# Kernel tuning notes

Measured on AMD Instinct MI355X. Metric: run time of the kernel, lower is better.

Reference implementation:

```python
import jax, jax.numpy as jnp
import numpy as np

BN_EPS = 1e-5

def setup_inputs() -> dict:
    key = jax.random.key(0)
    k1, k2, k3 = jax.random.split(key, 3)
    B, E, Cin, Cout, K, H, W = 32, 8, 64, 64, 3, 112, 112
    x = jax.random.normal(k1, (B, Cin, H, W), dtype=jnp.float32)
    routing_weight = jax.random.uniform(k2, (B, E), dtype=jnp.float32)
    experts = jax.random.normal(k3, (E, Cout, Cin, K, K), dtype=jnp.float32) * 0.05
    gamma = jnp.ones((Cout,), dtype=jnp.float32)
    beta = jnp.zeros((Cout,), dtype=jnp.float32)
    return {"x": x, "routing_weight": routing_weight, "experts": experts,
            "gamma": gamma, "beta": beta}

def reference(x, routing_weight, experts, gamma, beta):
    B, Cin, H, W = x.shape
    E, Cout, _, K, _ = experts.shape
    # Per-sample weighted combination of expert kernels: (B, Cout, Cin, K, K)
    kernels = jnp.einsum('be,eoihw->boihw', routing_weight, experts)
    # Batched conv via grouped-conv trick: groups = B
    xg = x.reshape(1, B * Cin, H, W)
    wg = kernels.reshape(B * Cout, Cin, K, K)
    pad = (K - 1) // 2
    out = jax.lax.conv_general_dilated(
        xg, wg,
        window_strides=(1, 1),
        padding=[(pad, pad), (pad, pad)],
        dimension_numbers=('NCHW', 'OIHW', 'NCHW'),
        feature_group_count=B,
    )
    out = out.reshape(B, Cout, H, W)
    # BatchNorm (training-mode batch stats, biased variance) + ReLU6
    mean = jnp.mean(out, axis=(0, 2, 3), keepdims=True)
    var = jnp.mean(jnp.square(out - mean), axis=(0, 2, 3), keepdims=True)
    g = gamma.reshape(1, -1, 1, 1)
    b = beta.reshape(1, -1, 1, 1)
    y = (out - mean) * jax.lax.rsqrt(var + BN_EPS) * g + b
    return jnp.clip(y, 0.0, 6.0)
```

## Files before the change

kernel.cpp:

```cpp
#include <hip/hip_runtime.h>
#include <stdint.h>

#define BN_EPS 1e-5f

typedef __attribute__((ext_vector_type(8))) short bf16x8;
typedef __attribute__((ext_vector_type(4))) float f32x4;

#define B_    32
#define E_    8
#define CIN   64
#define COUT  64
#define H_    112
#define W_    112
#define HW    (H_*W_)
#define HP    114
#define WP    114
#define CI    32
#define NCHUNK 2
#define NBLK  (B_*56)
#define XT_BC_BYTES (HP*WP*CI*2)
#define XT_BYTES    (B_*NCHUNK*XT_BC_BYTES)
#define KER_BC_BYTES (9*COUT*CI*2)
#define KER_OFF     XT_BYTES
#define KER_BYTES   (B_*NCHUNK*KER_BC_BYTES)
#define PART_OFF    (KER_OFF + KER_BYTES)
#define PART_BYTES  (NBLK*128*4)
#define STATS_OFF   (PART_OFF + PART_BYTES)
#define CVOUT_OFF   (STATS_OFF + 512)
#define CVOUT_BYTES ((long)B_*COUT*HW*2)
#define WS_NEED_BF16 (CVOUT_OFF + CVOUT_BYTES)

static __device__ __forceinline__ unsigned short f2bf(float f) {
    unsigned int u = __float_as_uint(f);
    unsigned int r = (u + 0x7fffu + ((u >> 16) & 1u)) >> 16;
    return (unsigned short)r;
}
static __device__ __forceinline__ float bf2f(unsigned short u) {
    return __uint_as_float(((unsigned int)u) << 16);
}

static __device__ __forceinline__ void gld16(void* lds, const void* g) {
    __builtin_amdgcn_global_load_lds(
        (const __attribute__((address_space(1))) void*)g,
        (__attribute__((address_space(3))) void*)lds, 16, 0, 0);
}

__global__ __launch_bounds__(256)
void prep_kernel(const float* __restrict__ rw,
                 const float* __restrict__ experts,
                 const float* __restrict__ x,
                 char* __restrict__ ws) {
    __shared__ float lds[16 * 289];
    int t = threadIdx.x;

    if (blockIdx.x < 256) {
        int blk = blockIdx.x;
        int oq  = blk & 3;
        int bc  = blk >> 2;
        int c = bc & 1, b = bc >> 1;

        float w[E_];
#pragma unroll
        for (int e = 0; e < E_; e++) w[e] = rw[b * E_ + e];

#pragma unroll
        for (int k = 0; k < 18; k++) {
            int idx = k * 256 + t;
            int o16 = idx / 288;
            int r   = idx - o16 * 288;
            long base = (long)(oq * 16 + o16) * 576 + c * 288 + r;
            float s = 0.f;
#pragma unroll
            for (int e = 0; e < E_; e++) s += w[e] * experts[(long)e * 36864 + base];
            lds[o16 * 289 + r] = s;
        }
        __syncthreads();

        char* kb = ws + (long)KER_OFF + (long)bc * KER_BC_BYTES;
        for (int u = t; u < 576; u += 256) {
            int slot = u & 3;
            int o16  = (u >> 2) & 15;
            int s    = u >> 6;
            float v[8];
#pragma unroll
            for (int j = 0; j < 8; j++) v[j] = lds[o16 * 289 + (slot * 8 + j) * 9 + s];
            uint4 p;
            p.x = (unsigned)f2bf(v[0]) | ((unsigned)f2bf(v[1]) << 16);
            p.y = (unsigned)f2bf(v[2]) | ((unsigned)f2bf(v[3]) << 16);
            p.z = (unsigned)f2bf(v[4]) | ((unsigned)f2bf(v[5]) << 16);
            p.w = (unsigned)f2bf(v[6]) | ((unsigned)f2bf(v[7]) << 16);
            *(uint4*)(kb + s * (COUT * CI * 2) + (oq * 16 + o16) * (CI * 2) + slot * 16) = p;
        }
    } else {
        int blk = blockIdx.x - 256;
        int hp  = blk % HP;
        int bc  = blk / HP;
        int c = bc & 1, b = bc >> 1;
        int h = hp - 1;
        bool border = (h < 0 || h >= H_);

        if (!border) {
            const float* src = x + ((long)(b * CIN + c * CI)) * HW + (long)h * W_;
#pragma unroll
            for (int idx = t; idx < 896; idx += 256) {
                int ch = idx / 28, col = idx % 28;
                float4 v = *(const float4*)(src + (long)ch * HW + col * 4);
                *(float4*)&lds[ch * 112 + col * 4] = v;
            }
        }
        __syncthreads();

        char* dst = ws + (long)bc * XT_BC_BYTES + (long)hp * (WP * CI * 2);
        for (int u = t; u < 456; u += 256) {
            int slot = u & 3, wp = u >> 2;
            int w = wp - 1;
            uint4 p = {0u, 0u, 0u, 0u};
            if (!border && w >= 0 && w < W_) {
                int ch0 = slot * 8;
                float v0 = lds[(ch0 + 0) * 112 + w], v1 = lds[(ch0 + 1) * 112 + w];
                float v2 = lds[(ch0 + 2) * 112 + w], v3 = lds[(ch0 + 3) * 112 + w];
                float v4 = lds[(ch0 + 4) * 112 + w], v5 = lds[(ch0 + 5) * 112 + w];
                float v6 = lds[(ch0 + 6) * 112 + w], v7 = lds[(ch0 + 7) * 112 + w];
                p.x = (unsigned)f2bf(v0) | ((unsigned)f2bf(v1) << 16);
                p.y = (unsigned)f2bf(v2) | ((unsigned)f2bf(v3) << 16);
                p.z = (unsigned)f2bf(v4) | ((unsigned)f2bf(v5) << 16);
                p.w = (unsigned)f2bf(v6) | ((unsigned)f2bf(v7) << 16);
            }
            int sw = slot ^ ((wp >> 1) & 3);
            *(uint4*)(dst + wp * 64 + sw * 16) = p;
        }
    }
}

template<bool BF16OUT>
__global__ __launch_bounds__(256)
void conv_kernel(const char* __restrict__ ws, void* __restrict__ outp,
                 float* __restrict__ partial) {
    __shared__ uint4 xs4[1888];
    char* xs = (char*)xs4;

    int blk0 = blockIdx.x;
    int blk  = (blk0 & 7) * 224 + (blk0 >> 3);
    int b  = blk / 56;
    int rb = blk % 56;
    int h0 = rb * 2;

    int tid  = threadIdx.x;
    int wave = tid >> 6;
    int lane = tid & 63;
    int l15  = lane & 15;
    int g    = lane >> 4;
    int row  = h0 + (wave >> 1);
    int obase = (wave & 1) * 32;
    int rhalf = wave >> 1;

    int swk[3];
#pragma unroll
    for (int kw = 0; kw < 3; kw++)
        swk[kw] = (g ^ (((l15 + kw) >> 1) & 3)) * 16 + (l15 + kw) * 64;

    f32x4 acc[7][2];
#pragma unroll
    for (int mt = 0; mt < 7; mt++)
#pragma unroll
        for (int nh = 0; nh < 2; nh++)
            acc[mt][nh] = (f32x4){0.f, 0.f, 0.f, 0.f};

    for (int c = 0; c < NCHUNK; c++) {
        int bc = b * 2 + c;
        if (c) __syncthreads();
        const char* src = ws + (long)bc * XT_BC_BYTES + (long)h0 * (WP * CI * 2);
#pragma unroll
        for (int i = 0; i < 7; i++) {
            int off = i * 4096 + wave * 1024;
            gld16(xs + off, src + off + lane * 16);
        }
        if (wave == 0) {
            int off = 7 * 4096;
            gld16(xs + off, src + off + lane * 16);
        }
        const char* kbase = ws + (long)KER_OFF + (long)bc * KER_BC_BYTES;
        bf16x8 bb[9][2];
#pragma unroll
        for (int s = 0; s < 9; s++)
#pragma unroll
            for (int nh = 0; nh < 2; nh++)
                bb[s][nh] = *(const bf16x8*)(kbase + (s * COUT + obase + nh * 16 + l15) * (CI * 2) + g * 16);
        __syncthreads();

#pragma unroll
        for (int s = 0; s < 9; s++) {
            const int kh = s / 3, kw = s % 3;
            const int base = (rhalf + kh) * (WP * 64) + swk[kw];
            bf16x8 a[7];
#pragma unroll
            for (int mt = 0; mt < 7; mt++)
                a[mt] = *(const bf16x8*)(xs + base + mt * 1024);
#pragma unroll
            for (int mt = 0; mt < 7; mt++)
#pragma unroll
                for (int nh = 0; nh < 2; nh++)
                    acc[mt][nh] = __builtin_amdgcn_mfma_f32_16x16x32_bf16(a[mt], bb[s][nh], acc[mt][nh], 0, 0, 0);
        }
    }

    float s1[2], s2[2];
#pragma unroll
    for (int nh = 0; nh < 2; nh++) {
        int o = obase + nh * 16 + l15;
        long base = ((long)(b * COUT + o) * H_ + row) * W_;
        s1[nh] = 0.f; s2[nh] = 0.f;
#pragma unroll
        for (int mt = 0; mt < 7; mt++) {
            if (BF16OUT) {
                unsigned short* cv = (unsigned short*)outp;
                uint2 pk;
                pk.x = (unsigned)f2bf(acc[mt][nh][0]) | ((unsigned)f2bf(acc[mt][nh][1]) << 16);
                pk.y = (unsigned)f2bf(acc[mt][nh][2]) | ((unsigned)f2bf(acc[mt][nh][3]) << 16);
                *(uint2*)(cv + base + mt * 16 + g * 4) = pk;
            } else {
                float* orow = (float*)outp + base;
                *(f32x4*)(orow + mt * 16 + g * 4) = acc[mt][nh];
            }
#pragma unroll
            for (int r = 0; r < 4; r++) {
                float v = acc[mt][nh][r];
                s1[nh] += v;
                s2[nh] += v * v;
            }
        }
        s1[nh] += __shfl_xor(s1[nh], 16, 64);
        s2[nh] += __shfl_xor(s2[nh], 16, 64);
        s1[nh] += __shfl_xor(s1[nh], 32, 64);
        s2[nh] += __shfl_xor(s2[nh], 32, 64);
    }

    __syncthreads();
    float* S = (float*)xs;
    if (g == 0) {
#pragma unroll
        for (int nh = 0; nh < 2; nh++) {
            S[wave * 64 +      nh * 16 + l15] = s1[nh];
            S[wave * 64 + 32 + nh * 16 + l15] = s2[nh];
        }
    }
    __syncthreads();
    if (tid < 128) {
        int stat = tid >> 6;
        int o    = tid & 63;
        int oh   = o >> 5;
        int o32  = o & 31;
        float v = S[oh * 64 + stat * 32 + o32] + S[(oh + 2) * 64 + stat * 32 + o32];
        partial[(long)blk * 128 + stat * 64 + o] = v;
    }
}

__global__ __launch_bounds__(1024)
void reduce_kernel(const float* __restrict__ partial, float* __restrict__ stats) {
    __shared__ float4 S[32][32];
    const float4* p4 = (const float4*)partial;
    int col4 = threadIdx.x & 31;
    int j    = threadIdx.x >> 5;
    float4 s = {0.f, 0.f, 0.f, 0.f};
#pragma unroll
    for (int k = 0; k < 56; k++) {
        float4 v = p4[(long)(k * 32 + j) * 32 + col4];
        s.x += v.x; s.y += v.y; s.z += v.z; s.w += v.w;
    }
    S[j][col4] = s;
    __syncthreads();
    if (threadIdx.x < 128) {
        int c4 = threadIdx.x & 31;
        int q0 = (threadIdx.x >> 5) * 8;
        float4 r = {0.f, 0.f, 0.f, 0.f};
#pragma unroll
        for (int q = 0; q < 8; q++) {
            float4 v = S[q0 + q][c4];
            r.x += v.x; r.y += v.y; r.z += v.z; r.w += v.w;
        }
        S[q0 / 8][c4] = r;
    }
    __syncthreads();
    if (threadIdx.x < 32) {
        float4 r = {0.f, 0.f, 0.f, 0.f};
#pragma unroll
        for (int q = 0; q < 4; q++) {
            float4 v = S[q][threadIdx.x];
            r.x += v.x; r.y += v.y; r.z += v.z; r.w += v.w;
        }
        ((float4*)stats)[threadIdx.x] = r;
    }
}

__global__ void bn_bf16_kernel(const unsigned short* __restrict__ cv, float* __restrict__ out,
                               const float* __restrict__ stats,
                               const float* __restrict__ gamma, const float* __restrict__ beta) {
    const float invN = 1.0f / ((float)B_ * HW);
    long i8 = (long)blockIdx.x * 256 + threadIdx.x;
    int o = (int)((i8 / (HW / 8)) & 63);
    float mean = stats[o] * invN;
    float var  = stats[COUT + o] * invN - mean * mean;
    float sc = gamma[o] * rsqrtf(var + BN_EPS);
    float sh = beta[o] - mean * sc;
    uint4 v = ((const uint4*)cv)[i8];
    float f[8];
    f[0] = bf2f((unsigned short)(v.x & 0xffff)); f[1] = bf2f((unsigned short)(v.x >> 16));
    f[2] = bf2f((unsigned short)(v.y & 0xffff)); f[3] = bf2f((unsigned short)(v.y >> 16));
    f[4] = bf2f((unsigned short)(v.z & 0xffff)); f[5] = bf2f((unsigned short)(v.z >> 16));
    f[6] = bf2f((unsigned short)(v.w & 0xffff)); f[7] = bf2f((unsigned short)(v.w >> 16));
    float4 o0, o1;
    o0.x = fminf(fmaxf(f[0] * sc + sh, 0.f), 6.f);
    o0.y = fminf(fmaxf(f[1] * sc + sh, 0.f), 6.f);
    o0.z = fminf(fmaxf(f[2] * sc + sh, 0.f), 6.f);
    o0.w = fminf(fmaxf(f[3] * sc + sh, 0.f), 6.f);
    o1.x = fminf(fmaxf(f[4] * sc + sh, 0.f), 6.f);
    o1.y = fminf(fmaxf(f[5] * sc + sh, 0.f), 6.f);
    o1.z = fminf(fmaxf(f[6] * sc + sh, 0.f), 6.f);
    o1.w = fminf(fmaxf(f[7] * sc + sh, 0.f), 6.f);
    ((float4*)out)[i8 * 2]     = o0;
    ((float4*)out)[i8 * 2 + 1] = o1;
}

__global__ void bn_kernel(float* __restrict__ out, const float* __restrict__ stats,
                          const float* __restrict__ gamma, const float* __restrict__ beta) {
    const float invN = 1.0f / ((float)B_ * HW);
    const long total4 = (long)B_ * COUT * HW / 4;
    for (long i4 = (long)blockIdx.x * 256 + threadIdx.x; i4 < total4;
         i4 += (long)gridDim.x * 256) {
        int o = (int)((i4 / (HW / 4)) & 63);
        float mean = stats[o] * invN;
        float var  = stats[COUT + o] * invN - mean * mean;
        float sc = gamma[o] * rsqrtf(var + BN_EPS);
        float sh = beta[o] - mean * sc;
        float4 v = ((float4*)out)[i4];
        v.x = fminf(fmaxf(v.x * sc + sh, 0.f), 6.f);
        v.y = fminf(fmaxf(v.y * sc + sh, 0.f), 6.f);
        v.z = fminf(fmaxf(v.z * sc + sh, 0.f), 6.f);
        v.w = fminf(fmaxf(v.w * sc + sh, 0.f), 6.f);
        ((float4*)out)[i4] = v;
    }
}

extern "C" void kernel_launch(void* const* d_in, const int* in_sizes, int n_in,
                              void* d_out, int out_size, void* d_ws, size_t ws_size,
                              hipStream_t stream) {
    const float* x       = (const float*)d_in[0];
    const float* rw      = (const float*)d_in[1];
    const float* experts = (const float*)d_in[2];
    const float* gamma   = (const float*)d_in[3];
    const float* beta    = (const float*)d_in[4];
    float* out = (float*)d_out;
    char*  ws  = (char*)d_ws;
    float* partial = (float*)(ws + PART_OFF);
    float* stats   = (float*)(ws + STATS_OFF);

    prep_kernel<<<256 + B_ * NCHUNK * HP, 256, 0, stream>>>(rw, experts, x, ws);

    if (ws_size >= (size_t)WS_NEED_BF16) {
        unsigned short* cv = (unsigned short*)(ws + CVOUT_OFF);
        conv_kernel<true><<<NBLK, 256, 0, stream>>>(ws, (void*)cv, partial);
        reduce_kernel<<<1, 1024, 0, stream>>>(partial, stats);
        bn_bf16_kernel<<<12544, 256, 0, stream>>>(cv, out, stats, gamma, beta);
    } else {
        conv_kernel<false><<<NBLK, 256, 0, stream>>>(ws, (void*)out, partial);
        reduce_kernel<<<1, 1024, 0, stream>>>(partial, stats);
        bn_kernel<<<4096, 256, 0, stream>>>(out, stats, gamma, beta);
    }
}
```

Baseline: 116.8 us.

## Double-buffer input channel chunks in LDS to overlap loads with MFMA

```diff
diff --git a/kernel.cpp b/kernel.cpp
--- a/kernel.cpp
+++ b/kernel.cpp
@@ -45,6 +45,19 @@
         (__attribute__((address_space(3))) void*)lds, 16, 0, 0);
 }
 
+static __device__ __forceinline__ void stage_rows(char* dst, const char* src,
+                                                  int wave, int lane) {
+#pragma unroll
+    for (int i = 0; i < 7; i++) {
+        int off = i * 4096 + wave * 1024;
+        gld16(dst + off, src + off + lane * 16);
+    }
+    if (wave == 0) {
+        int off = 7 * 4096;
+        gld16(dst + off, src + off + lane * 16);
+    }
+}
+
 __global__ __launch_bounds__(256)
 void prep_kernel(const float* __restrict__ rw,
                  const float* __restrict__ experts,
@@ -136,8 +149,8 @@
 __global__ __launch_bounds__(256)
 void conv_kernel(const char* __restrict__ ws, void* __restrict__ outp,
                  float* __restrict__ partial) {
-    __shared__ uint4 xs4[1888];
-    char* xs = (char*)xs4;
+    __shared__ uint4 xs4[2][1856];
+    char* xsbuf[2] = {(char*)xs4[0], (char*)xs4[1]};
 
     int blk0 = blockIdx.x;
     int blk  = (blk0 & 7) * 224 + (blk0 >> 3);
@@ -166,28 +179,49 @@
         for (int nh = 0; nh < 2; nh++)
             acc[mt][nh] = (f32x4){0.f, 0.f, 0.f, 0.f};
 
-    for (int c = 0; c < NCHUNK; c++) {
-        int bc = b * 2 + c;
-        if (c) __syncthreads();
-        const char* src = ws + (long)bc * XT_BC_BYTES + (long)h0 * (WP * CI * 2);
-#pragma unroll
-        for (int i = 0; i < 7; i++) {
-            int off = i * 4096 + wave * 1024;
-            gld16(xs + off, src + off + lane * 16);
-        }
-        if (wave == 0) {
-            int off = 7 * 4096;
-            gld16(xs + off, src + off + lane * 16);
-        }
-        const char* kbase = ws + (long)KER_OFF + (long)bc * KER_BC_BYTES;
-        bf16x8 bb[9][2];
-#pragma unroll
-        for (int s = 0; s < 9; s++)
-#pragma unroll
-            for (int nh = 0; nh < 2; nh++)
-                bb[s][nh] = *(const bf16x8*)(kbase + (s * COUT + obase + nh * 16 + l15) * (CI * 2) + g * 16);
-        __syncthreads();
-
+    const char* src0 = ws + (long)(b * 2 + 0) * XT_BC_BYTES + (long)h0 * (WP * CI * 2);
+    const char* src1 = ws + (long)(b * 2 + 1) * XT_BC_BYTES + (long)h0 * (WP * CI * 2);
+    const char* kbase0 = ws + (long)KER_OFF + (long)(b * 2 + 0) * KER_BC_BYTES;
+    const char* kbase1 = kbase0 + KER_BC_BYTES;
+
+    stage_rows(xsbuf[0], src0, wave, lane);
+    __syncthreads();
+
+    bf16x8 bb[9][2];
+#pragma unroll
+    for (int s = 0; s < 9; s++)
+#pragma unroll
+        for (int nh = 0; nh < 2; nh++)
+            bb[s][nh] = *(const bf16x8*)(kbase0 + (s * COUT + obase + nh * 16 + l15) * (CI * 2) + g * 16);
+
+    stage_rows(xsbuf[1], src1, wave, lane);
+
+    {
+        char* xs = xsbuf[0];
+#pragma unroll
+        for (int s = 0; s < 9; s++) {
+            const int kh = s / 3, kw = s % 3;
+            const int base = (rhalf + kh) * (WP * 64) + swk[kw];
+            bf16x8 a[7];
+#pragma unroll
+            for (int mt = 0; mt < 7; mt++)
+                a[mt] = *(const bf16x8*)(xs + base + mt * 1024);
+#pragma unroll
+            for (int mt = 0; mt < 7; mt++)
+#pragma unroll
+                for (int nh = 0; nh < 2; nh++)
+                    acc[mt][nh] = __builtin_amdgcn_mfma_f32_16x16x32_bf16(a[mt], bb[s][nh], acc[mt][nh], 0, 0, 0);
+        }
+    }
+    __syncthreads();
+
+#pragma unroll
+    for (int s = 0; s < 9; s++)
+#pragma unroll
+        for (int nh = 0; nh < 2; nh++)
+            bb[s][nh] = *(const bf16x8*)(kbase1 + (s * COUT + obase + nh * 16 + l15) * (CI * 2) + g * 16);
+    {
+        char* xs = xsbuf[1];
 #pragma unroll
         for (int s = 0; s < 9; s++) {
             const int kh = s / 3, kw = s % 3;
@@ -236,7 +270,7 @@
     }
 
     __syncthreads();
-    float* S = (float*)xs;
+    float* S = (float*)xs4;
     if (g == 0) {
 #pragma unroll
         for (int nh = 0; nh < 2; nh++) {
```

Result: no change. 116.9 us (+0.1%).
